# Performance work log

Measured on AMD Instinct MI355X. Metric: run time of the kernel, lower is better.

The kernel has to match this reference:

```python
import jax, jax.numpy as jnp
import numpy as np

N = 16384      # num_nodes
E = 524288     # num_edges (avg degree 32)
B = 32         # batch_size
D = 64         # input_dim
OUT = 64       # output_dim
K = 2          # max_diffusion_step
M = 2 * K + 1  # num_matrices = len(supports)*K + 1


def setup_inputs() -> dict:
    key = jax.random.key(0)
    k1, k2, k3, k4, k5 = jax.random.split(key, 5)
    inputs = jax.random.normal(k1, (B, N, D), dtype=jnp.float32)
    rows = jax.random.randint(k2, (E,), 0, N)
    cols = jax.random.randint(k3, (E,), 0, N)
    adj_vals = jax.random.uniform(k4, (E,), dtype=jnp.float32)
    # xavier_normal_ init for weights [D*M, OUT]
    std = (2.0 / (D * M + OUT)) ** 0.5
    weights = jax.random.normal(k5, (D * M, OUT), dtype=jnp.float32) * std
    biases = jnp.zeros((1, OUT), dtype=jnp.float32)  # bias_start = 0.0
    return dict(inputs=inputs, adj_vals=adj_vals, rows=rows, cols=cols,
                weights=weights, biases=biases)


def _spmm(vals, src, dst, x):
    # y[dst] += vals * x[src]; x: [N, F]  (sparse matrix-vector over edge list)
    return jax.ops.segment_sum(vals[:, None] * x[src], dst, num_segments=N)


def reference(inputs, adj_vals, rows, cols, weights, biases):
    b, n, d = inputs.shape
    # calculate_random_walk_matrix(A) = D_row^{-1} A ; support1 = its transpose
    # calculate_random_walk_matrix(A^T) = D_col^{-1} A^T ; support2 = its transpose
    drow = jax.ops.segment_sum(adj_vals, rows, num_segments=N)
    dcol = jax.ops.segment_sum(adj_vals, cols, num_segments=N)
    inv_drow = jnp.where(drow > 0, 1.0 / drow, 0.0)
    inv_dcol = jnp.where(dcol > 0, 1.0 / dcol, 0.0)
    vals1 = adj_vals * inv_drow[rows]  # support1 @ x: gather src=rows, scatter dst=cols
    vals2 = adj_vals * inv_dcol[cols]  # support2 @ x: gather src=cols, scatter dst=rows
    supports = [(vals1, rows, cols), (vals2, cols, rows)]

    # x0 layout: permute(1,2,0) -> [N, D, B] -> [N, D*B]
    x0 = jnp.transpose(inputs, (1, 2, 0)).reshape(n, d * b)
    xs = [x0]
    for vals, src, dst in supports:
        x1 = _spmm(vals, src, dst, x0)
        xs.append(x1)
        for _ in range(2, K + 1):
            x2 = 2.0 * _spmm(vals, src, dst, x1) - x0
            xs.append(x2)
            x1, x0 = x2, x1  # NOTE: x0 deliberately NOT reset between supports (matches torch src)
    x = jnp.stack(xs, axis=0).reshape(M, n, d, b)       # [M, N, D, B]
    x = jnp.transpose(x, (3, 1, 2, 0)).reshape(b * n, d * M)  # [B*N, D*M]
    out = x @ weights + biases
    return out.reshape(b, n, OUT)
```

## Files before the change

kernel.cpp:

```cpp
#include <hip/hip_runtime.h>
#include <stdint.h>

#define NN 16384
#define EE 524288
#define BB 32
#define DD 64
#define OO 64
#define MM 5
#define KK 320

typedef __attribute__((ext_vector_type(2))) _Float16 half2_t;
typedef __attribute__((ext_vector_type(8))) _Float16 half8_t;
typedef __attribute__((ext_vector_type(4))) float floatx4;

__global__ __launch_bounds__(256) void hist_kernel(
    const float* __restrict__ adj, const int* __restrict__ rows,
    const int* __restrict__ cols,
    float* __restrict__ drow, float* __restrict__ dcol,
    int* __restrict__ cnt_row, int* __restrict__ cnt_col)
{
    int e = blockIdx.x * 256 + threadIdx.x;
    if (e < EE) {
        float a = adj[e];
        int r = rows[e], c = cols[e];
        atomicAdd(&drow[r], a);
        atomicAdd(&dcol[c], a);
        atomicAdd(&cnt_row[r], 1);
        atomicAdd(&cnt_col[c], 1);
    }
}

__global__ __launch_bounds__(1024) void scan_kernel(
    const int* __restrict__ cnt_col, const int* __restrict__ cnt_row,
    int* __restrict__ off_col, int* __restrict__ off_row,
    int* __restrict__ cur_col, int* __restrict__ cur_row)
{
    const int* cnt = (blockIdx.x == 0) ? cnt_col : cnt_row;
    int* off = (blockIdx.x == 0) ? off_col : off_row;
    int* cur = (blockIdx.x == 0) ? cur_col : cur_row;

    __shared__ int part[1024];
    int t = threadIdx.x;
    int base = t * 16;
    int local[16];
    int s = 0;
#pragma unroll
    for (int i = 0; i < 16; i++) { local[i] = cnt[base + i]; s += local[i]; }
    part[t] = s;
    __syncthreads();
    for (int d = 1; d < 1024; d <<= 1) {
        int v = (t >= d) ? part[t - d] : 0;
        __syncthreads();
        part[t] += v;
        __syncthreads();
    }
    int run = (t == 0) ? 0 : part[t - 1];
#pragma unroll
    for (int i = 0; i < 16; i++) {
        off[base + i] = run;
        cur[base + i] = run;
        run += local[i];
    }
    if (t == 1023) off[NN] = run;
}

__global__ __launch_bounds__(1024) void degsort_kernel(
    const int* __restrict__ off_col, const int* __restrict__ off_row,
    int* __restrict__ perm_col, int* __restrict__ perm_row)
{
    const int* off = (blockIdx.x == 0) ? off_col : off_row;
    int* perm = (blockIdx.x == 0) ? perm_col : perm_row;

    __shared__ int bins[512];
    __shared__ int cur[512];
    int t = threadIdx.x;
    if (t < 512) bins[t] = 0;
    __syncthreads();
    for (int i = t; i < NN; i += 1024) {
        int d = off[i + 1] - off[i];
        if (d > 511) d = 511;
        atomicAdd(&bins[d], 1);
    }
    __syncthreads();
    for (int sh = 1; sh < 512; sh <<= 1) {
        int v = (t < 512 && t >= sh) ? bins[t - sh] : 0;
        __syncthreads();
        if (t < 512) bins[t] += v;
        __syncthreads();
    }
    if (t < 512) cur[t] = (t == 0) ? 0 : bins[t - 1];
    __syncthreads();
    for (int i = t; i < NN; i += 1024) {
        int d = off[i + 1] - off[i];
        if (d > 511) d = 511;
        int p = atomicAdd(&cur[d], 1);
        perm[p] = i;
    }
}

__global__ __launch_bounds__(256) void scatter_kernel(
    const float* __restrict__ adj, const int* __restrict__ rows,
    const int* __restrict__ cols,
    const float* __restrict__ drow, const float* __restrict__ dcol,
    int* __restrict__ cur_col, int* __restrict__ cur_row,
    int2* __restrict__ edge1, int2* __restrict__ edge2)
{
    int e = blockIdx.x * 256 + threadIdx.x;
    if (e < EE) {
        float a = adj[e];
        int r = rows[e], c = cols[e];
        float dr = drow[r];
        float idr = (dr > 0.f) ? (1.f / dr) : 0.f;
        float dc = dcol[c];
        float idc = (dc > 0.f) ? (1.f / dc) : 0.f;
        _Float16 h1 = (_Float16)(a * idr);
        _Float16 h2 = (_Float16)(a * idc);
        unsigned short u1 = __builtin_bit_cast(unsigned short, h1);
        unsigned short u2 = __builtin_bit_cast(unsigned short, h2);
        int p1 = atomicAdd(&cur_col[c], 1);
        edge1[p1] = make_int2(r, (int)(u1 | ((unsigned int)u1 << 16)));
        int p2 = atomicAdd(&cur_row[r], 1);
        edge2[p2] = make_int2(c, (int)(u2 | ((unsigned int)u2 << 16)));
    }
}

__global__ __launch_bounds__(256) void cast_kernel(
    const float* __restrict__ inp, unsigned short* __restrict__ x0)
{
    size_t i = ((size_t)blockIdx.x * 256 + threadIdx.x) * 8;
    float4 a = *(const float4*)(inp + i);
    float4 b = *(const float4*)(inp + i + 4);
    half2_t h0 = {(_Float16)a.x, (_Float16)a.y};
    half2_t h1 = {(_Float16)a.z, (_Float16)a.w};
    half2_t h2 = {(_Float16)b.x, (_Float16)b.y};
    half2_t h3 = {(_Float16)b.z, (_Float16)b.w};
    uint4 o;
    o.x = __builtin_bit_cast(unsigned int, h0);
    o.y = __builtin_bit_cast(unsigned int, h1);
    o.z = __builtin_bit_cast(unsigned int, h2);
    o.w = __builtin_bit_cast(unsigned int, h3);
    *(uint4*)(x0 + i) = o;
}

__global__ __launch_bounds__(256) void wprep_kernel(
    const float* __restrict__ W, unsigned short* __restrict__ Wt)
{
    int i = blockIdx.x * 256 + threadIdx.x;
    if (i < OO * KK) {
        int o = i / KK;
        int kp = i - o * KK;
        int m = kp >> 6;
        int d = kp & 63;
        _Float16 h = (_Float16)W[(d * MM + m) * OO + o];
        Wt[i] = __builtin_bit_cast(unsigned short, h);
    }
}

__global__ __launch_bounds__(256) void spmm_kernel(
    const unsigned short* __restrict__ xin,
    const unsigned short* __restrict__ z,
    unsigned short* __restrict__ xout,
    const int* __restrict__ off, const int* __restrict__ perm,
    const int2* __restrict__ edges,
    float alpha, float beta, int has_z)
{
    unsigned int l = blockIdx.x;
    int xcd  = l & 7;
    unsigned int s = l >> 3;
    int bhi  = s >> 9;
    int ntile = s & 511;
    int b = bhi * 8 + xcd;

    int t = threadIdx.x;
    int n = perm[ntile * 32 + (t >> 3)];
    unsigned int dgb = (unsigned int)(t & 7) * 16u;
    int e0 = off[n], e1 = off[n + 1];
    const char* xbB = (const char*)(xin + (size_t)b * NN * DD);

    half2_t acc0 = (half2_t)0, acc1 = (half2_t)0, acc2 = (half2_t)0, acc3 = (half2_t)0;

#define GATHER(ED) (*(const uint4*)(xbB + (((unsigned int)(ED).x) << 7) + dgb))
#define FMA4(V, W2)                                                       \
    do {                                                                  \
        acc0 = __builtin_bit_cast(half2_t, (V).x) * (W2) + acc0;          \
        acc1 = __builtin_bit_cast(half2_t, (V).y) * (W2) + acc1;          \
        acc2 = __builtin_bit_cast(half2_t, (V).z) * (W2) + acc2;          \
        acc3 = __builtin_bit_cast(half2_t, (V).w) * (W2) + acc3;          \
    } while (0)

    int ecnt = e1 - e0;
    int nb8 = ecnt >> 3;

    int2 ed0, ed1, ed2, ed3, ed4, ed5, ed6, ed7;
    if (nb8 > 0) {
        ed0 = edges[e0];     ed1 = edges[e0 + 1];
        ed2 = edges[e0 + 2]; ed3 = edges[e0 + 3];
        ed4 = edges[e0 + 4]; ed5 = edges[e0 + 5];
        ed6 = edges[e0 + 6]; ed7 = edges[e0 + 7];
    }
    for (int it = 0; it < nb8; ++it) {
        uint4 v0 = GATHER(ed0);
        uint4 v1 = GATHER(ed1);
        uint4 v2 = GATHER(ed2);
        uint4 v3 = GATHER(ed3);
        uint4 v4 = GATHER(ed4);
        uint4 v5 = GATHER(ed5);
        uint4 v6 = GATHER(ed6);
        uint4 v7 = GATHER(ed7);
        half2_t w0 = __builtin_bit_cast(half2_t, ed0.y);
        half2_t w1 = __builtin_bit_cast(half2_t, ed1.y);
        half2_t w2 = __builtin_bit_cast(half2_t, ed2.y);
        half2_t w3 = __builtin_bit_cast(half2_t, ed3.y);
        half2_t w4 = __builtin_bit_cast(half2_t, ed4.y);
        half2_t w5 = __builtin_bit_cast(half2_t, ed5.y);
        half2_t w6 = __builtin_bit_cast(half2_t, ed6.y);
        half2_t w7 = __builtin_bit_cast(half2_t, ed7.y);

        int ep = (it + 1 < nb8) ? (e0 + (it + 1) * 8) : e0;
        int2 nd0 = edges[ep];     int2 nd1 = edges[ep + 1];
        int2 nd2 = edges[ep + 2]; int2 nd3 = edges[ep + 3];
        int2 nd4 = edges[ep + 4]; int2 nd5 = edges[ep + 5];
        int2 nd6 = edges[ep + 6]; int2 nd7 = edges[ep + 7];

        FMA4(v0, w0);
        FMA4(v1, w1);
        FMA4(v2, w2);
        FMA4(v3, w3);
        FMA4(v4, w4);
        FMA4(v5, w5);
        FMA4(v6, w6);
        FMA4(v7, w7);

        ed0 = nd0; ed1 = nd1; ed2 = nd2; ed3 = nd3;
        ed4 = nd4; ed5 = nd5; ed6 = nd6; ed7 = nd7;
    }
    for (int e = e0 + nb8 * 8; e < e1; ++e) {
        int2 ed = edges[e];
        half2_t wv = __builtin_bit_cast(half2_t, ed.y);
        uint4 v = GATHER(ed);
        FMA4(v, wv);
    }
#undef FMA4
#undef GATHER

    size_t fo = ((size_t)b * NN + n) * DD + (dgb >> 1);
    if (has_z) {
        uint4 zv = *(const uint4*)(z + fo);
        half2_t al = {(_Float16)alpha, (_Float16)alpha};
        half2_t be = {(_Float16)beta, (_Float16)beta};
        acc0 = al * acc0 + be * __builtin_bit_cast(half2_t, zv.x);
        acc1 = al * acc1 + be * __builtin_bit_cast(half2_t, zv.y);
        acc2 = al * acc2 + be * __builtin_bit_cast(half2_t, zv.z);
        acc3 = al * acc3 + be * __builtin_bit_cast(half2_t, zv.w);
    }

    uint4 o;
    o.x = __builtin_bit_cast(unsigned int, acc0);
    o.y = __builtin_bit_cast(unsigned int, acc1);
    o.z = __builtin_bit_cast(unsigned int, acc2);
    o.w = __builtin_bit_cast(unsigned int, acc3);
    *(uint4*)(xout + fo) = o;
}

__global__ __launch_bounds__(256, 4) void final_mfma(
    const unsigned short* __restrict__ X0, const unsigned short* __restrict__ X1,
    const unsigned short* __restrict__ X2, const unsigned short* __restrict__ X3,
    const unsigned short* __restrict__ X4,
    const unsigned short* __restrict__ Wt, const float* __restrict__ bias,
    float* __restrict__ out)
{
    int blk = blockIdx.x;
    int b = blk >> 6;
    int n0 = (blk & 63) * 256;
    int t = threadIdx.x;
    int wave = t >> 6;
    int lane = t & 63;
    int col = lane & 15;
    int quad = lane >> 4;

    size_t rowbase = (size_t)b * NN + n0 + wave * 64;

    floatx4 acc[4][4];
#pragma unroll
    for (int ct = 0; ct < 4; ct++)
#pragma unroll
        for (int rt = 0; rt < 4; rt++) acc[ct][rt] = (floatx4){0.f, 0.f, 0.f, 0.f};

#define KSTEP(XP, m, h)                                                          \
    {                                                                            \
        const unsigned short* xa = (XP) + rowbase * DD + (h) * 32 + quad * 8;    \
        half8_t a0 = *(const half8_t*)(xa + (0 * 16 + col) * DD);                \
        half8_t a1 = *(const half8_t*)(xa + (1 * 16 + col) * DD);                \
        half8_t a2 = *(const half8_t*)(xa + (2 * 16 + col) * DD);                \
        half8_t a3 = *(const half8_t*)(xa + (3 * 16 + col) * DD);                \
        const unsigned short* wb = Wt + ((m) * 2 + (h)) * 32 + quad * 8;         \
        half8_t b0 = *(const half8_t*)(wb + (0 * 16 + col) * KK);                \
        half8_t b1 = *(const half8_t*)(wb + (1 * 16 + col) * KK);                \
        half8_t b2 = *(const half8_t*)(wb + (2 * 16 + col) * KK);                \
        half8_t b3 = *(const half8_t*)(wb + (3 * 16 + col) * KK);                \
        acc[0][0] = __builtin_amdgcn_mfma_f32_16x16x32_f16(a0, b0, acc[0][0], 0, 0, 0); \
        acc[0][1] = __builtin_amdgcn_mfma_f32_16x16x32_f16(a1, b0, acc[0][1], 0, 0, 0); \
        acc[0][2] = __builtin_amdgcn_mfma_f32_16x16x32_f16(a2, b0, acc[0][2], 0, 0, 0); \
        acc[0][3] = __builtin_amdgcn_mfma_f32_16x16x32_f16(a3, b0, acc[0][3], 0, 0, 0); \
        acc[1][0] = __builtin_amdgcn_mfma_f32_16x16x32_f16(a0, b1, acc[1][0], 0, 0, 0); \
        acc[1][1] = __builtin_amdgcn_mfma_f32_16x16x32_f16(a1, b1, acc[1][1], 0, 0, 0); \
        acc[1][2] = __builtin_amdgcn_mfma_f32_16x16x32_f16(a2, b1, acc[1][2], 0, 0, 0); \
        acc[1][3] = __builtin_amdgcn_mfma_f32_16x16x32_f16(a3, b1, acc[1][3], 0, 0, 0); \
        acc[2][0] = __builtin_amdgcn_mfma_f32_16x16x32_f16(a0, b2, acc[2][0], 0, 0, 0); \
        acc[2][1] = __builtin_amdgcn_mfma_f32_16x16x32_f16(a1, b2, acc[2][1], 0, 0, 0); \
        acc[2][2] = __builtin_amdgcn_mfma_f32_16x16x32_f16(a2, b2, acc[2][2], 0, 0, 0); \
        acc[2][3] = __builtin_amdgcn_mfma_f32_16x16x32_f16(a3, b2, acc[2][3], 0, 0, 0); \
        acc[3][0] = __builtin_amdgcn_mfma_f32_16x16x32_f16(a0, b3, acc[3][0], 0, 0, 0); \
        acc[3][1] = __builtin_amdgcn_mfma_f32_16x16x32_f16(a1, b3, acc[3][1], 0, 0, 0); \
        acc[3][2] = __builtin_amdgcn_mfma_f32_16x16x32_f16(a2, b3, acc[3][2], 0, 0, 0); \
        acc[3][3] = __builtin_amdgcn_mfma_f32_16x16x32_f16(a3, b3, acc[3][3], 0, 0, 0); \
    }

    KSTEP(X0, 0, 0)
    KSTEP(X0, 0, 1)
    KSTEP(X1, 1, 0)
    KSTEP(X1, 1, 1)
    KSTEP(X2, 2, 0)
    KSTEP(X2, 2, 1)
    KSTEP(X3, 3, 0)
    KSTEP(X3, 3, 1)
    KSTEP(X4, 4, 0)
    KSTEP(X4, 4, 1)
#undef KSTEP

#pragma unroll
    for (int ct = 0; ct < 4; ct++) {
        int o = ct * 16 + col;
        float bv = bias[o];
#pragma unroll
        for (int rt = 0; rt < 4; rt++) {
            size_t rb = rowbase + rt * 16 + quad * 4;
#pragma unroll
            for (int r = 0; r < 4; r++) {
                out[(rb + r) * OO + o] = acc[ct][rt][r] + bv;
            }
        }
    }
}

extern "C" void kernel_launch(void* const* d_in, const int* in_sizes, int n_in,
                              void* d_out, int out_size, void* d_ws, size_t ws_size,
                              hipStream_t stream)
{
    (void)in_sizes; (void)n_in; (void)out_size; (void)ws_size;
    const float* inputs  = (const float*)d_in[0];
    const float* adj     = (const float*)d_in[1];
    const int*   rows    = (const int*)d_in[2];
    const int*   cols    = (const int*)d_in[3];
    const float* weights = (const float*)d_in[4];
    const float* bias    = (const float*)d_in[5];
    float* out = (float*)d_out;

    char* ws = (char*)d_ws;
    size_t off = 0;
    auto alloc = [&](size_t bytes) -> char* {
        char* p = ws + off;
        off = (off + bytes + 255) & ~(size_t)255;
        return p;
    };
    float* drow    = (float*)alloc(NN * 4);
    float* dcol    = (float*)alloc(NN * 4);
    int* cnt_col   = (int*)alloc(NN * 4);
    int* cnt_row   = (int*)alloc(NN * 4);
    int* off_col   = (int*)alloc((NN + 1) * 4);
    int* off_row   = (int*)alloc((NN + 1) * 4);
    int* cur_col   = (int*)alloc(NN * 4);
    int* cur_row   = (int*)alloc(NN * 4);
    int* perm_col  = (int*)alloc(NN * 4);
    int* perm_row  = (int*)alloc(NN * 4);
    int2* edge1    = (int2*)alloc((size_t)EE * 8);
    int2* edge2    = (int2*)alloc((size_t)EE * 8);
    unsigned short* Wt = (unsigned short*)alloc((size_t)OO * KK * 2);
    unsigned short* X[MM];
    for (int m = 0; m < MM; m++) X[m] = (unsigned short*)alloc((size_t)NN * BB * DD * 2);

    hipMemsetAsync(drow, 0, (size_t)NN * 4 * 4, stream);

    hist_kernel<<<EE / 256, 256, 0, stream>>>(adj, rows, cols, drow, dcol,
                                              cnt_row, cnt_col);
    scan_kernel<<<2, 1024, 0, stream>>>(cnt_col, cnt_row, off_col, off_row,
                                        cur_col, cur_row);
    degsort_kernel<<<2, 1024, 0, stream>>>(off_col, off_row, perm_col, perm_row);
    scatter_kernel<<<EE / 256, 256, 0, stream>>>(adj, rows, cols, drow, dcol,
                                                 cur_col, cur_row, edge1, edge2);
    cast_kernel<<<(BB * NN * DD) / (256 * 8), 256, 0, stream>>>(inputs, X[0]);
    wprep_kernel<<<(OO * KK + 255) / 256, 256, 0, stream>>>(weights, Wt);

    const int SPMM_GRID = 512 * BB;

    spmm_kernel<<<SPMM_GRID, 256, 0, stream>>>(X[0], nullptr, X[1], off_col,
                                               perm_col, edge1, 1.f, 0.f, 0);
    spmm_kernel<<<SPMM_GRID, 256, 0, stream>>>(X[1], X[0], X[2], off_col,
                                               perm_col, edge1, 2.f, -1.f, 1);
    spmm_kernel<<<SPMM_GRID, 256, 0, stream>>>(X[1], nullptr, X[3], off_row,
                                               perm_row, edge2, 1.f, 0.f, 0);
    spmm_kernel<<<SPMM_GRID, 256, 0, stream>>>(X[3], X[1], X[4], off_row,
                                               perm_row, edge2, 2.f, -1.f, 1);

    final_mfma<<<BB * (NN / 256), 256, 0, stream>>>(X[0], X[1], X[2], X[3], X[4],
                                                    Wt, bias, out);
}
```

Measured before the change: 1.025 ms.

## Fuse preprocessing kernels, merge independent SpMMs, and shrink final GEMM tile

Merges the histogram, cast and weight-prep kernels into one launch, and the degree sort and edge scatter into another, cutting launch count and serial gaps. The second support-1 SpMM and the first support-2 SpMM both read X1, so they now run in one dual launch that doubles the grid and gives more parallel work. SpMM specializes has_z via a template. The final MFMA kernel tiles 128 rows per block with half the accumulators and a higher occupancy hint, at the cost of reloading weight fragments more often.

New measurement: 1.021 ms. About the same (-0.4%).

```diff
diff --git a/kernel.cpp b/kernel.cpp
--- a/kernel.cpp
+++ b/kernel.cpp
@@ -9,24 +9,57 @@
 #define MM 5
 #define KK 320
 
+#define HIST_BLKS  (EE / 256)
+#define CAST_BLKS  ((BB * NN * DD) / (256 * 8))
+#define WPREP_BLKS ((OO * KK + 255) / 256)
+#define SPMM_GRID  (512 * BB)
+
 typedef __attribute__((ext_vector_type(2))) _Float16 half2_t;
 typedef __attribute__((ext_vector_type(8))) _Float16 half8_t;
 typedef __attribute__((ext_vector_type(4))) float floatx4;
 
-__global__ __launch_bounds__(256) void hist_kernel(
+__global__ __launch_bounds__(256) void fused_pre(
+    const float* __restrict__ inp, unsigned short* __restrict__ x0,
     const float* __restrict__ adj, const int* __restrict__ rows,
     const int* __restrict__ cols,
     float* __restrict__ drow, float* __restrict__ dcol,
-    int* __restrict__ cnt_row, int* __restrict__ cnt_col)
-{
-    int e = blockIdx.x * 256 + threadIdx.x;
-    if (e < EE) {
+    int* __restrict__ cnt_row, int* __restrict__ cnt_col,
+    const float* __restrict__ W, unsigned short* __restrict__ Wt)
+{
+    unsigned int blk = blockIdx.x;
+    int t = threadIdx.x;
+    if (blk < HIST_BLKS) {
+        int e = blk * 256 + t;
         float a = adj[e];
         int r = rows[e], c = cols[e];
         atomicAdd(&drow[r], a);
         atomicAdd(&dcol[c], a);
         atomicAdd(&cnt_row[r], 1);
         atomicAdd(&cnt_col[c], 1);
+    } else if (blk < HIST_BLKS + CAST_BLKS) {
+        size_t i = ((size_t)(blk - HIST_BLKS) * 256 + t) * 8;
+        float4 a = *(const float4*)(inp + i);
+        float4 b = *(const float4*)(inp + i + 4);
+        half2_t h0 = {(_Float16)a.x, (_Float16)a.y};
+        half2_t h1 = {(_Float16)a.z, (_Float16)a.w};
+        half2_t h2 = {(_Float16)b.x, (_Float16)b.y};
+        half2_t h3 = {(_Float16)b.z, (_Float16)b.w};
+        uint4 o;
+        o.x = __builtin_bit_cast(unsigned int, h0);
+        o.y = __builtin_bit_cast(unsigned int, h1);
+        o.z = __builtin_bit_cast(unsigned int, h2);
+        o.w = __builtin_bit_cast(unsigned int, h3);
+        *(uint4*)(x0 + i) = o;
+    } else {
+        int i = (blk - HIST_BLKS - CAST_BLKS) * 256 + t;
+        if (i < OO * KK) {
+            int o = i / KK;
+            int kp = i - o * KK;
+            int m = kp >> 6;
+            int d = kp & 63;
+            _Float16 h = (_Float16)W[(d * MM + m) * OO + o];
+            Wt[i] = __builtin_bit_cast(unsigned short, h);
+        }
     }
 }
 
@@ -64,107 +97,75 @@
     if (t == 1023) off[NN] = run;
 }
 
-__global__ __launch_bounds__(1024) void degsort_kernel(
+__global__ __launch_bounds__(1024) void fused_build(
     const int* __restrict__ off_col, const int* __restrict__ off_row,
-    int* __restrict__ perm_col, int* __restrict__ perm_row)
-{
-    const int* off = (blockIdx.x == 0) ? off_col : off_row;
-    int* perm = (blockIdx.x == 0) ? perm_col : perm_row;
-
-    __shared__ int bins[512];
-    __shared__ int cur[512];
-    int t = threadIdx.x;
-    if (t < 512) bins[t] = 0;
-    __syncthreads();
-    for (int i = t; i < NN; i += 1024) {
-        int d = off[i + 1] - off[i];
-        if (d > 511) d = 511;
-        atomicAdd(&bins[d], 1);
-    }
-    __syncthreads();
-    for (int sh = 1; sh < 512; sh <<= 1) {
-        int v = (t < 512 && t >= sh) ? bins[t - sh] : 0;
-        __syncthreads();
-        if (t < 512) bins[t] += v;
-        __syncthreads();
-    }
-    if (t < 512) cur[t] = (t == 0) ? 0 : bins[t - 1];
-    __syncthreads();
-    for (int i = t; i < NN; i += 1024) {
-        int d = off[i + 1] - off[i];
-        if (d > 511) d = 511;
-        int p = atomicAdd(&cur[d], 1);
-        perm[p] = i;
-    }
-}
-
-__global__ __launch_bounds__(256) void scatter_kernel(
+    int* __restrict__ perm_col, int* __restrict__ perm_row,
     const float* __restrict__ adj, const int* __restrict__ rows,
     const int* __restrict__ cols,
     const float* __restrict__ drow, const float* __restrict__ dcol,
     int* __restrict__ cur_col, int* __restrict__ cur_row,
     int2* __restrict__ edge1, int2* __restrict__ edge2)
 {
-    int e = blockIdx.x * 256 + threadIdx.x;
-    if (e < EE) {
-        float a = adj[e];
-        int r = rows[e], c = cols[e];
-        float dr = drow[r];
-        float idr = (dr > 0.f) ? (1.f / dr) : 0.f;
-        float dc = dcol[c];
-        float idc = (dc > 0.f) ? (1.f / dc) : 0.f;
-        _Float16 h1 = (_Float16)(a * idr);
-        _Float16 h2 = (_Float16)(a * idc);
-        unsigned short u1 = __builtin_bit_cast(unsigned short, h1);
-        unsigned short u2 = __builtin_bit_cast(unsigned short, h2);
-        int p1 = atomicAdd(&cur_col[c], 1);
-        edge1[p1] = make_int2(r, (int)(u1 | ((unsigned int)u1 << 16)));
-        int p2 = atomicAdd(&cur_row[r], 1);
-        edge2[p2] = make_int2(c, (int)(u2 | ((unsigned int)u2 << 16)));
-    }
-}
-
-__global__ __launch_bounds__(256) void cast_kernel(
-    const float* __restrict__ inp, unsigned short* __restrict__ x0)
-{
-    size_t i = ((size_t)blockIdx.x * 256 + threadIdx.x) * 8;
-    float4 a = *(const float4*)(inp + i);
-    float4 b = *(const float4*)(inp + i + 4);
-    half2_t h0 = {(_Float16)a.x, (_Float16)a.y};
-    half2_t h1 = {(_Float16)a.z, (_Float16)a.w};
-    half2_t h2 = {(_Float16)b.x, (_Float16)b.y};
-    half2_t h3 = {(_Float16)b.z, (_Float16)b.w};
-    uint4 o;
-    o.x = __builtin_bit_cast(unsigned int, h0);
-    o.y = __builtin_bit_cast(unsigned int, h1);
-    o.z = __builtin_bit_cast(unsigned int, h2);
-    o.w = __builtin_bit_cast(unsigned int, h3);
-    *(uint4*)(x0 + i) = o;
-}
-
-__global__ __launch_bounds__(256) void wprep_kernel(
-    const float* __restrict__ W, unsigned short* __restrict__ Wt)
-{
-    int i = blockIdx.x * 256 + threadIdx.x;
-    if (i < OO * KK) {
-        int o = i / KK;
-        int kp = i - o * KK;
-        int m = kp >> 6;
-        int d = kp & 63;
-        _Float16 h = (_Float16)W[(d * MM + m) * OO + o];
-        Wt[i] = __builtin_bit_cast(unsigned short, h);
-    }
-}
-
-__global__ __launch_bounds__(256) void spmm_kernel(
+    unsigned int blk = blockIdx.x;
+    int t = threadIdx.x;
+    if (blk < 2) {
+        const int* off = (blk == 0) ? off_col : off_row;
+        int* perm = (blk == 0) ? perm_col : perm_row;
+        __shared__ int bins[512];
+        __shared__ int cur[512];
+        if (t < 512) bins[t] = 0;
+        __syncthreads();
+        for (int i = t; i < NN; i += 1024) {
+            int d = off[i + 1] - off[i];
+            if (d > 511) d = 511;
+            atomicAdd(&bins[d], 1);
+        }
+        __syncthreads();
+        for (int sh = 1; sh < 512; sh <<= 1) {
+            int v = (t < 512 && t >= sh) ? bins[t - sh] : 0;
+            __syncthreads();
+            if (t < 512) bins[t] += v;
+            __syncthreads();
+        }
+        if (t < 512) cur[t] = (t == 0) ? 0 : bins[t - 1];
+        __syncthreads();
+        for (int i = t; i < NN; i += 1024) {
+            int d = off[i + 1] - off[i];
+            if (d > 511) d = 511;
+            int p = atomicAdd(&cur[d], 1);
+            perm[p] = i;
+        }
+    } else {
+        int e = (blk - 2) * 1024 + t;
+        if (e < EE) {
+            float a = adj[e];
+            int r = rows[e], c = cols[e];
+            float dr = drow[r];
+            float idr = (dr > 0.f) ? (1.f / dr) : 0.f;
+            float dc = dcol[c];
+            float idc = (dc > 0.f) ? (1.f / dc) : 0.f;
+            _Float16 h1 = (_Float16)(a * idr);
+            _Float16 h2 = (_Float16)(a * idc);
+            unsigned short u1 = __builtin_bit_cast(unsigned short, h1);
+            unsigned short u2 = __builtin_bit_cast(unsigned short, h2);
+            int p1 = atomicAdd(&cur_col[c], 1);
+            edge1[p1] = make_int2(r, (int)(u1 | ((unsigned int)u1 << 16)));
+            int p2 = atomicAdd(&cur_row[r], 1);
+            edge2[p2] = make_int2(c, (int)(u2 | ((unsigned int)u2 << 16)));
+        }
+    }
+}
+
+template<int HAS_Z>
+__device__ __forceinline__ void spmm_body(
+    unsigned int l,
     const unsigned short* __restrict__ xin,
     const unsigned short* __restrict__ z,
     unsigned short* __restrict__ xout,
     const int* __restrict__ off, const int* __restrict__ perm,
     const int2* __restrict__ edges,
-    float alpha, float beta, int has_z)
-{
-    unsigned int l = blockIdx.x;
+    float alpha, float beta)
+{
     int xcd  = l & 7;
     unsigned int s = l >> 3;
     int bhi  = s >> 9;
@@ -244,7 +245,7 @@
 #undef GATHER
 
     size_t fo = ((size_t)b * NN + n) * DD + (dgb >> 1);
-    if (has_z) {
+    if (HAS_Z) {
         uint4 zv = *(const uint4*)(z + fo);
         half2_t al = {(_Float16)alpha, (_Float16)alpha};
         half2_t be = {(_Float16)beta, (_Float16)beta};
@@ -262,7 +263,35 @@
     *(uint4*)(xout + fo) = o;
 }
 
-__global__ __launch_bounds__(256, 4) void final_mfma(
+template<int HAS_Z>
+__global__ __launch_bounds__(256) void spmm_kernel(
+    const unsigned short* __restrict__ xin,
+    const unsigned short* __restrict__ z,
+    unsigned short* __restrict__ xout,
+    const int* __restrict__ off, const int* __restrict__ perm,
+    const int2* __restrict__ edges,
+    float alpha, float beta)
+{
+    spmm_body<HAS_Z>(blockIdx.x, xin, z, xout, off, perm, edges, alpha, beta);
+}
+
+__global__ __launch_bounds__(256) void spmm_dual(
+    const unsigned short* __restrict__ X0, const unsigned short* __restrict__ X1,
+    unsigned short* __restrict__ X2, unsigned short* __restrict__ X3,
+    const int* __restrict__ off_col, const int* __restrict__ perm_col,
+    const int2* __restrict__ edge1,
+    const int* __restrict__ off_row, const int* __restrict__ perm_row,
+    const int2* __restrict__ edge2)
+{
+    unsigned int blk = blockIdx.x;
+    if (blk < SPMM_GRID) {
+        spmm_body<1>(blk, X1, X0, X2, off_col, perm_col, edge1, 2.f, -1.f);
+    } else {
+        spmm_body<0>(blk - SPMM_GRID, X1, nullptr, X3, off_row, perm_row, edge2, 1.f, 0.f);
+    }
+}
+
+__global__ __launch_bounds__(256, 5) void final_mfma(
     const unsigned short* __restrict__ X0, const unsigned short* __restrict__ X1,
     const unsigned short* __restrict__ X2, const unsigned short* __restrict__ X3,
     const unsigned short* __restrict__ X4,
@@ -270,29 +299,27 @@
     float* __restrict__ out)
 {
     int blk = blockIdx.x;
-    int b = blk >> 6;
-    int n0 = (blk & 63) * 256;
+    int b = blk >> 7;
+    int n0 = (blk & 127) * 128;
     int t = threadIdx.x;
     int wave = t >> 6;
     int lane = t & 63;
     int col = lane & 15;
     int quad = lane >> 4;
 
-    size_t rowbase = (size_t)b * NN + n0 + wave * 64;
-
-    floatx4 acc[4][4];
+    size_t rowbase = (size_t)b * NN + n0 + wave * 32;
+
+    floatx4 acc[4][2];
 #pragma unroll
     for (int ct = 0; ct < 4; ct++)
 #pragma unroll
-        for (int rt = 0; rt < 4; rt++) acc[ct][rt] = (floatx4){0.f, 0.f, 0.f, 0.f};
+        for (int rt = 0; rt < 2; rt++) acc[ct][rt] = (floatx4){0.f, 0.f, 0.f, 0.f};
 
 #define KSTEP(XP, m, h)                                                          \
     {                                                                            \
         const unsigned short* xa = (XP) + rowbase * DD + (h) * 32 + quad * 8;    \
         half8_t a0 = *(const half8_t*)(xa + (0 * 16 + col) * DD);                \
         half8_t a1 = *(const half8_t*)(xa + (1 * 16 + col) * DD);                \
-        half8_t a2 = *(const half8_t*)(xa + (2 * 16 + col) * DD);                \
-        half8_t a3 = *(const half8_t*)(xa + (3 * 16 + col) * DD);                \
         const unsigned short* wb = Wt + ((m) * 2 + (h)) * 32 + quad * 8;         \
         half8_t b0 = *(const half8_t*)(wb + (0 * 16 + col) * KK);                \
         half8_t b1 = *(const half8_t*)(wb + (1 * 16 + col) * KK);                \
@@ -300,20 +327,12 @@
         half8_t b3 = *(const half8_t*)(wb + (3 * 16 + col) * KK);                \
         acc[0][0] = __builtin_amdgcn_mfma_f32_16x16x32_f16(a0, b0, acc[0][0], 0, 0, 0); \
         acc[0][1] = __builtin_amdgcn_mfma_f32_16x16x32_f16(a1, b0, acc[0][1], 0, 0, 0); \
-        acc[0][2] = __builtin_amdgcn_mfma_f32_16x16x32_f16(a2, b0, acc[0][2], 0, 0, 0); \
-        acc[0][3] = __builtin_amdgcn_mfma_f32_16x16x32_f16(a3, b0, acc[0][3], 0, 0, 0); \
         acc[1][0] = __builtin_amdgcn_mfma_f32_16x16x32_f16(a0, b1, acc[1][0], 0, 0, 0); \
         acc[1][1] = __builtin_amdgcn_mfma_f32_16x16x32_f16(a1, b1, acc[1][1], 0, 0, 0); \
-        acc[1][2] = __builtin_amdgcn_mfma_f32_16x16x32_f16(a2, b1, acc[1][2], 0, 0, 0); \
-        acc[1][3] = __builtin_amdgcn_mfma_f32_16x16x32_f16(a3, b1, acc[1][3], 0, 0, 0); \
         acc[2][0] = __builtin_amdgcn_mfma_f32_16x16x32_f16(a0, b2, acc[2][0], 0, 0, 0); \
         acc[2][1] = __builtin_amdgcn_mfma_f32_16x16x32_f16(a1, b2, acc[2][1], 0, 0, 0); \
-        acc[2][2] = __builtin_amdgcn_mfma_f32_16x16x32_f16(a2, b2, acc[2][2], 0, 0, 0); \
-        acc[2][3] = __builtin_amdgcn_mfma_f32_16x16x32_f16(a3, b2, acc[2][3], 0, 0, 0); \
         acc[3][0] = __builtin_amdgcn_mfma_f32_16x16x32_f16(a0, b3, acc[3][0], 0, 0, 0); \
         acc[3][1] = __builtin_amdgcn_mfma_f32_16x16x32_f16(a1, b3, acc[3][1], 0, 0, 0); \
-        acc[3][2] = __builtin_amdgcn_mfma_f32_16x16x32_f16(a2, b3, acc[3][2], 0, 0, 0); \
-        acc[3][3] = __builtin_amdgcn_mfma_f32_16x16x32_f16(a3, b3, acc[3][3], 0, 0, 0); \
     }
 
     KSTEP(X0, 0, 0)
@@ -333,7 +352,7 @@
         int o = ct * 16 + col;
         float bv = bias[o];
 #pragma unroll
-        for (int rt = 0; rt < 4; rt++) {
+        for (int rt = 0; rt < 2; rt++) {
             size_t rb = rowbase + rt * 16 + quad * 4;
 #pragma unroll
             for (int r = 0; r < 4; r++) {
@@ -381,27 +400,23 @@
 
     hipMemsetAsync(drow, 0, (size_t)NN * 4 * 4, stream);
 
-    hist_kernel<<<EE / 256, 256, 0, stream>>>(adj, rows, cols, drow, dcol,
-                                              cnt_row, cnt_col);
+    fused_pre<<<HIST_BLKS + CAST_BLKS + WPREP_BLKS, 256, 0, stream>>>(
+        inputs, X[0], adj, rows, cols, drow, dcol, cnt_row, cnt_col,
+        weights, Wt);
     scan_kernel<<<2, 1024, 0, stream>>>(cnt_col, cnt_row, off_col, off_row,
                                         cur_col, cur_row);
-    degsort_kernel<<<2, 1024, 0, stream>>>(off_col, off_row, perm_col, perm_row);
-    scatter_kernel<<<EE / 256, 256, 0, stream>>>(adj, rows, cols, drow, dcol,
-                                                 cur_col, cur_row, edge1, edge2);
-    cast_kernel<<<(BB * NN * DD) / (256 * 8), 256, 0, stream>>>(inputs, X[0]);
-    wprep_kernel<<<(OO * KK + 255) / 256, 256, 0, stream>>>(weights, Wt);
-
-    const int SPMM_GRID = 512 * BB;
-
-    spmm_kernel<<<SPMM_GRID, 256, 0, stream>>>(X[0], nullptr, X[1], off_col,
-                                               perm_col, edge1, 1.f, 0.f, 0);
-    spmm_kernel<<<SPMM_GRID, 256, 0, stream>>>(X[1], X[0], X[2], off_col,
-                                               perm_col, edge1, 2.f, -1.f, 1);
-    spmm_kernel<<<SPMM_GRID, 256, 0, stream>>>(X[1], nullptr, X[3], off_row,
-                                               perm_row, edge2, 1.f, 0.f, 0);
-    spmm_kernel<<<SPMM_GRID, 256, 0, stream>>>(X[3], X[1], X[4], off_row,
-                                               perm_row, edge2, 2.f, -1.f, 1);
-
-    final_mfma<<<BB * (NN / 256), 256, 0, stream>>>(X[0], X[1], X[2], X[3], X[4],
+    fused_build<<<2 + EE / 1024, 1024, 0, stream>>>(
+        off_col, off_row, perm_col, perm_row,
+        adj, rows, cols, drow, dcol, cur_col, cur_row, edge1, edge2);
+
+    spmm_kernel<0><<<SPMM_GRID, 256, 0, stream>>>(X[0], nullptr, X[1], off_col,
+                                                  perm_col, edge1, 1.f, 0.f);
+    spmm_dual<<<2 * SPMM_GRID, 256, 0, stream>>>(X[0], X[1], X[2], X[3],
+                                                 off_col, perm_col, edge1,
+                                                 off_row, perm_row, edge2);
+    spmm_kernel<1><<<SPMM_GRID, 256, 0, stream>>>(X[3], X[1], X[4], off_row,
+                                                  perm_row, edge2, 2.f, -1.f);
+
+    final_mfma<<<BB * (NN / 128), 256, 0, stream>>>(X[0], X[1], X[2], X[3], X[4],
                                                     Wt, bias, out);
 }
```
